# Optimization experiments

Measured on AMD Instinct MI355X. Metric: run time of the kernel, lower is better.

## Reference

```python
import jax, jax.numpy as jnp
import numpy as np

STATE_DIM = 15


def setup_inputs() -> dict:
    key = jax.random.key(0)
    k1, k2, k3 = jax.random.split(key, 3)
    B, S = 4096, 128
    dba_params = jax.random.normal(k1, (B, S, 32), dtype=jnp.float32)
    imu_measurements = jax.random.normal(k2, (B, S, 6), dtype=jnp.float32)
    gt_state = jax.random.normal(k3, (B, S, STATE_DIM), dtype=jnp.float32)
    return {"dba_params": dba_params, "imu_measurements": imu_measurements, "gt_state": gt_state}


def reference(dba_params, imu_measurements, gt_state):
    # use_gt_init=True path: initial pose (pos + quat) taken from gt_state[:, 0, :7]
    B, S, _ = dba_params.shape
    delta = dba_params[..., :7] * 0.1          # [B, S, 7]
    init_pos = gt_state[:, 0, 0:3]              # [B, 3]
    init_q = gt_state[:, 0, 3:7]                # [B, 4]

    # Positions: pure cumulative sum of deltas (no normalization).
    pos = jnp.concatenate(
        [init_pos[:, None, :],
         init_pos[:, None, :] + jnp.cumsum(delta[:, : S - 1, 0:3], axis=1)],
        axis=1)                                 # [B, S, 3]

    # Quaternions: sequential add + renormalize each step -> lax.scan over S-1.
    def step(q, dq):
        new_q = q + dq
        new_q = new_q / jnp.linalg.norm(new_q, axis=-1, keepdims=True)
        return new_q, new_q

    dq_seq = jnp.swapaxes(delta[:, : S - 1, 3:7], 0, 1)  # [S-1, B, 4]
    _, q_steps = jax.lax.scan(step, init_q, dq_seq)       # [S-1, B, 4]
    quats = jnp.concatenate([init_q[:, None, :], jnp.swapaxes(q_steps, 0, 1)], axis=1)  # [B, S, 4]

    rest = jnp.zeros((B, S, STATE_DIM - 7), dtype=dba_params.dtype)  # channels 7:15 stay zero
    return jnp.concatenate([pos, quats, rest], axis=-1)  # [B, S, 15]
```

## Files before the change

kernel.cpp:

```cpp
#include <hip/hip_runtime.h>

#define SEQ 128
#define SD  15
#define REC 32
#define WPB 4
#define NT  (WPB * 64)

__global__ __launch_bounds__(NT, 4) void fused_kernel(const float* __restrict__ dba,
                                                      const float* __restrict__ gt,
                                                      float* __restrict__ out,
                                                      int B) {
    const int tid  = threadIdx.x;
    const int wave = tid >> 6;
    const int lane = tid & 63;
    const int r    = blockIdx.x * WPB + wave;
    if (r >= B) return;

    __shared__ float4 sdq [WPB][SEQ];
    __shared__ float  pack[WPB][SEQ * SD];

    const float* rec0 = dba + ((size_t)r * SEQ + 2 * lane) * REC;
    const float4 h0a = *reinterpret_cast<const float4*>(rec0);
    const float4 h0b = *reinterpret_cast<const float4*>(rec0 + 4);
    const float4 h1a = *reinterpret_cast<const float4*>(rec0 + REC);
    const float4 h1b = *reinterpret_cast<const float4*>(rec0 + REC + 4);
    const float* g   = gt + (size_t)r * SEQ * SD;
    const float4 gA  = *reinterpret_cast<const float4*>(g);
    const float4 gB  = *reinterpret_cast<const float4*>(g + 4);

    sdq[wave][2 * lane]     = make_float4(h0a.w * 0.1f, h0b.x * 0.1f,
                                          h0b.y * 0.1f, h0b.z * 0.1f);
    sdq[wave][2 * lane + 1] = make_float4(h1a.w * 0.1f, h1b.x * 0.1f,
                                          h1b.y * 0.1f, h1b.z * 0.1f);

    const float d0x = h0a.x * 0.1f, d0y = h0a.y * 0.1f, d0z = h0a.z * 0.1f;
    const float d1x = h1a.x * 0.1f, d1y = h1a.y * 0.1f, d1z = h1a.z * 0.1f;

    const float sx = d0x + d1x, sy = d0y + d1y, sz = d0z + d1z;
    float ix = sx, iy = sy, iz = sz;
#pragma unroll
    for (int off = 1; off < 64; off <<= 1) {
        const float tx = __shfl_up(ix, off, 64);
        const float ty = __shfl_up(iy, off, 64);
        const float tz = __shfl_up(iz, off, 64);
        if (lane >= off) { ix += tx; iy += ty; iz += tz; }
    }
    const float ex = ix - sx, ey = iy - sy, ez = iz - sz;

    float* pw = pack[wave];
    {
        float* p0 = pw + (2 * lane) * SD;
        p0[0] = gA.x + ex; p0[1] = gA.y + ey; p0[2] = gA.z + ez;
#pragma unroll
        for (int k = 7; k < SD; ++k) p0[k] = 0.f;
        float* p1 = p0 + SD;
        p1[0] = gA.x + ex + d0x; p1[1] = gA.y + ey + d0y; p1[2] = gA.z + ez + d0z;
#pragma unroll
        for (int k = 7; k < SD; ++k) p1[k] = 0.f;
        if (lane == 0) {
            pw[3] = gA.w; pw[4] = gB.x; pw[5] = gB.y; pw[6] = gB.z;
        }
    }

    asm volatile("s_waitcnt lgkmcnt(0)" ::: "memory");

    if (lane == 0) {
        const float4* srow = sdq[wave];
        float* qp = pw + SD + 3;
        float q0 = gA.w, q1 = gB.x, q2 = gB.y, q3 = gB.z;

#define QSTEP(C) do {                                                   \
            q0 += (C).x; q1 += (C).y; q2 += (C).z; q3 += (C).w;         \
            const float a_ = q0 * q0 + q1 * q1;                         \
            const float b_ = q2 * q2 + q3 * q3;                         \
            const float i_ = __builtin_amdgcn_rsqf(a_ + b_);            \
            q0 *= i_; q1 *= i_; q2 *= i_; q3 *= i_;                     \
            qp[0] = q0; qp[1] = q1; qp[2] = q2; qp[3] = q3;             \
            qp += SD;                                                   \
        } while (0)

        float4 c0 = srow[0], c1 = srow[1], c2 = srow[2], c3 = srow[3],
               c4 = srow[4], c5 = srow[5], c6 = srow[6], c7 = srow[7];
        for (int w = 0; w < 15; ++w) {
            const float4* nx = srow + (w + 1) * 8;
            const float4 n0 = nx[0], n1 = nx[1], n2 = nx[2], n3 = nx[3],
                         n4 = nx[4], n5 = nx[5], n6 = nx[6], n7 = nx[7];
            QSTEP(c0); QSTEP(c1); QSTEP(c2); QSTEP(c3);
            QSTEP(c4); QSTEP(c5); QSTEP(c6); QSTEP(c7);
            c0 = n0; c1 = n1; c2 = n2; c3 = n3;
            c4 = n4; c5 = n5; c6 = n6; c7 = n7;
        }
        QSTEP(c0); QSTEP(c1); QSTEP(c2); QSTEP(c3);
        QSTEP(c4); QSTEP(c5); QSTEP(c6);
#undef QSTEP
    }

    asm volatile("s_waitcnt lgkmcnt(0)" ::: "memory");

    float4* o4 = reinterpret_cast<float4*>(out + (size_t)r * SEQ * SD);
    const float4* s4 = reinterpret_cast<const float4*>(pw);
#pragma unroll
    for (int k = lane; k < SEQ * SD / 4; k += 64)
        o4[k] = s4[k];
}

extern "C" void kernel_launch(void* const* d_in, const int* in_sizes, int n_in,
                              void* d_out, int out_size, void* d_ws, size_t ws_size,
                              hipStream_t stream) {
    const float* dba = (const float*)d_in[0];
    const float* gt  = (const float*)d_in[2];
    float* out = (float*)d_out;

    const int B = in_sizes[0] / (SEQ * REC);
    const int blocks = (B + WPB - 1) / WPB;
    fused_kernel<<<blocks, NT, 0, stream>>>(dba, gt, out, B);
}
```

Before: 32.23 us.

## Write outputs directly to global, stage only quaternions in LDS, raise occupancy

```diff
diff --git a/kernel.cpp b/kernel.cpp
--- a/kernel.cpp
+++ b/kernel.cpp
@@ -6,7 +6,7 @@
 #define WPB 4
 #define NT  (WPB * 64)
 
-__global__ __launch_bounds__(NT, 4) void fused_kernel(const float* __restrict__ dba,
+__global__ __launch_bounds__(NT, 8) void fused_kernel(const float* __restrict__ dba,
                                                       const float* __restrict__ gt,
                                                       float* __restrict__ out,
                                                       int B) {
@@ -16,17 +16,18 @@
     const int r    = blockIdx.x * WPB + wave;
     if (r >= B) return;
 
-    __shared__ float4 sdq [WPB][SEQ];
-    __shared__ float  pack[WPB][SEQ * SD];
+    __shared__ float4 sdq  [WPB][SEQ + 1];
+    __shared__ float4 squat[WPB][SEQ + 1];
+
+    const float* g  = gt + (size_t)r * SEQ * SD;
+    const float4 gA = *reinterpret_cast<const float4*>(g);
+    const float4 gB = *reinterpret_cast<const float4*>(g + 4);
 
     const float* rec0 = dba + ((size_t)r * SEQ + 2 * lane) * REC;
     const float4 h0a = *reinterpret_cast<const float4*>(rec0);
     const float4 h0b = *reinterpret_cast<const float4*>(rec0 + 4);
     const float4 h1a = *reinterpret_cast<const float4*>(rec0 + REC);
     const float4 h1b = *reinterpret_cast<const float4*>(rec0 + REC + 4);
-    const float* g   = gt + (size_t)r * SEQ * SD;
-    const float4 gA  = *reinterpret_cast<const float4*>(g);
-    const float4 gB  = *reinterpret_cast<const float4*>(g + 4);
 
     sdq[wave][2 * lane]     = make_float4(h0a.w * 0.1f, h0b.x * 0.1f,
                                           h0b.y * 0.1f, h0b.z * 0.1f);
@@ -47,61 +48,56 @@
     }
     const float ex = ix - sx, ey = iy - sy, ez = iz - sz;
 
-    float* pw = pack[wave];
-    {
-        float* p0 = pw + (2 * lane) * SD;
-        p0[0] = gA.x + ex; p0[1] = gA.y + ey; p0[2] = gA.z + ez;
+    float* o0 = out + ((size_t)r * SEQ + 2 * lane) * SD;
+    o0[0] = gA.x + ex; o0[1] = gA.y + ey; o0[2] = gA.z + ez;
+    if (lane == 0) {
+        o0[3] = gA.w; o0[4] = gB.x; o0[5] = gB.y; o0[6] = gB.z;
+    }
 #pragma unroll
-        for (int k = 7; k < SD; ++k) p0[k] = 0.f;
-        float* p1 = p0 + SD;
-        p1[0] = gA.x + ex + d0x; p1[1] = gA.y + ey + d0y; p1[2] = gA.z + ez + d0z;
+    for (int k = 7; k < SD; ++k) o0[k] = 0.f;
+    float* o1 = o0 + SD;
+    o1[0] = gA.x + ex + d0x; o1[1] = gA.y + ey + d0y; o1[2] = gA.z + ez + d0z;
 #pragma unroll
-        for (int k = 7; k < SD; ++k) p1[k] = 0.f;
-        if (lane == 0) {
-            pw[3] = gA.w; pw[4] = gB.x; pw[5] = gB.y; pw[6] = gB.z;
-        }
-    }
+    for (int k = 7; k < SD; ++k) o1[k] = 0.f;
 
     asm volatile("s_waitcnt lgkmcnt(0)" ::: "memory");
 
     if (lane == 0) {
         const float4* srow = sdq[wave];
-        float* qp = pw + SD + 3;
+        float4*       qrow = squat[wave];
         float q0 = gA.w, q1 = gB.x, q2 = gB.y, q3 = gB.z;
 
-#define QSTEP(C) do {                                                   \
+#define QSTEP(C, T) do {                                                \
             q0 += (C).x; q1 += (C).y; q2 += (C).z; q3 += (C).w;         \
             const float a_ = q0 * q0 + q1 * q1;                         \
             const float b_ = q2 * q2 + q3 * q3;                         \
             const float i_ = __builtin_amdgcn_rsqf(a_ + b_);            \
             q0 *= i_; q1 *= i_; q2 *= i_; q3 *= i_;                     \
-            qp[0] = q0; qp[1] = q1; qp[2] = q2; qp[3] = q3;             \
-            qp += SD;                                                   \
+            qrow[T] = make_float4(q0, q1, q2, q3);                      \
         } while (0)
 
-        float4 c0 = srow[0], c1 = srow[1], c2 = srow[2], c3 = srow[3],
-               c4 = srow[4], c5 = srow[5], c6 = srow[6], c7 = srow[7];
-        for (int w = 0; w < 15; ++w) {
-            const float4* nx = srow + (w + 1) * 8;
-            const float4 n0 = nx[0], n1 = nx[1], n2 = nx[2], n3 = nx[3],
-                         n4 = nx[4], n5 = nx[5], n6 = nx[6], n7 = nx[7];
-            QSTEP(c0); QSTEP(c1); QSTEP(c2); QSTEP(c3);
-            QSTEP(c4); QSTEP(c5); QSTEP(c6); QSTEP(c7);
+        float4 c0 = srow[0], c1 = srow[1], c2 = srow[2], c3 = srow[3];
+        for (int w = 0; w < 31; ++w) {
+            const float4* nx = srow + (w + 1) * 4;
+            const float4 n0 = nx[0], n1 = nx[1], n2 = nx[2], n3 = nx[3];
+            const int t = w * 4 + 1;
+            QSTEP(c0, t); QSTEP(c1, t + 1); QSTEP(c2, t + 2); QSTEP(c3, t + 3);
             c0 = n0; c1 = n1; c2 = n2; c3 = n3;
-            c4 = n4; c5 = n5; c6 = n6; c7 = n7;
         }
-        QSTEP(c0); QSTEP(c1); QSTEP(c2); QSTEP(c3);
-        QSTEP(c4); QSTEP(c5); QSTEP(c6);
+        QSTEP(c0, 125); QSTEP(c1, 126); QSTEP(c2, 127);
 #undef QSTEP
     }
 
     asm volatile("s_waitcnt lgkmcnt(0)" ::: "memory");
 
-    float4* o4 = reinterpret_cast<float4*>(out + (size_t)r * SEQ * SD);
-    const float4* s4 = reinterpret_cast<const float4*>(pw);
-#pragma unroll
-    for (int k = lane; k < SEQ * SD / 4; k += 64)
-        o4[k] = s4[k];
+    if (lane > 0) {
+        const float4 q = squat[wave][2 * lane];
+        o0[3] = q.x; o0[4] = q.y; o0[5] = q.z; o0[6] = q.w;
+    }
+    {
+        const float4 q = squat[wave][2 * lane + 1];
+        o1[3] = q.x; o1[4] = q.y; o1[5] = q.z; o1[6] = q.w;
+    }
 }
 
 extern "C" void kernel_launch(void* const* d_in, const int* in_sizes, int n_in,
```

Result: slower. 36.91 us (+14.5%).
